# Kernel tuning notes

Hardware: AMD Instinct MI355X
Metric: run time of the kernel (lower is better)

## Reference

```python
import jax, jax.numpy as jnp
import numpy as np

B, L, S, H, C = 64, 512, 512, 768, 9  # batch, bert subword len, word seq len, hidden, num_classes


def setup_inputs() -> dict:
    key = jax.random.key(0)
    k1, k2, k3 = jax.random.split(key, 3)
    rng = np.random.RandomState(0)
    # per-word subword counts in {1,2,3}; truncate so totals fit in L subword slots
    lens = rng.randint(1, 4, size=(B, S))
    cum = lens.cumsum(axis=1)
    keep = cum <= L
    ids_lens = (lens * keep).astype(np.int32)
    totals = ids_lens.sum(axis=1)
    attention_mask = (np.arange(L)[None, :] < totals[:, None]).astype(np.int32)
    label_mask = ids_lens > 0
    label_ids = (rng.randint(0, C, size=(B, S)) * label_mask).astype(np.int32)
    bert_out = jax.random.normal(k1, (B, L, H), dtype=jnp.float32)
    W = jax.random.normal(k2, (H, C), dtype=jnp.float32) * 0.02
    b = jnp.zeros((C,), dtype=jnp.float32)
    return {
        "bert_out": bert_out,
        "W": W,
        "b": b,
        "attention_mask": jnp.asarray(attention_mask),
        "ids_lens": jnp.asarray(ids_lens),
        "label_ids": jnp.asarray(label_ids),
        "label_mask": jnp.asarray(label_mask),
    }


def reference(bert_out, W, b, attention_mask, ids_lens, label_ids, label_mask):
    Bv, Lv, Hv = bert_out.shape
    Sv = ids_lens.shape[1]
    nseg = Bv * Sv
    am = attention_mask.astype(jnp.int32)
    # subword position within each example's valid region
    sidx = jnp.cumsum(am, axis=1) - 1                       # [B, L]
    # word index for each subword: searchsorted into cumulative word lengths
    ends = jnp.cumsum(ids_lens, axis=1)                     # [B, S]
    widx = jax.vmap(lambda e, s: jnp.searchsorted(e, s, side='right'))(ends, sidx)
    seg = jnp.where(am > 0, widx + jnp.arange(Bv)[:, None] * Sv, nseg)  # pad bucket = nseg
    flat = bert_out.reshape(Bv * Lv, Hv)
    segf = seg.reshape(Bv * Lv)
    sums = jax.ops.segment_sum(flat, segf, num_segments=nseg + 1)[:nseg]
    cnts = jax.ops.segment_sum(jnp.ones((Bv * Lv,), bert_out.dtype), segf,
                               num_segments=nseg + 1)[:nseg]
    mean = sums / jnp.maximum(cnts, 1.0)[:, None]           # segment mean (split().mean(0))
    word_mask = (ids_lens > 0).reshape(nseg)
    embed = jnp.where(word_mask[:, None], mean, 0.0).reshape(Bv, Sv, Hv)  # masked_scatter
    # dropout in eval mode = identity
    logits = embed @ W + b                                  # [B, S, C]
    logp = jax.nn.log_softmax(logits, axis=-1)
    lab = jnp.clip(label_ids, 0, W.shape[1] - 1)
    nll = -jnp.take_along_axis(logp, lab[..., None].astype(jnp.int32), axis=-1)[..., 0]
    valid = label_mask.astype(bert_out.dtype)
    loss = jnp.sum(nll * valid) / jnp.maximum(jnp.sum(valid), 1.0)
    pred = jnp.argmax(logits, axis=-1)
    return loss, pred
```

## Files before the change

kernel.cpp:

```cpp
#include <hip/hip_runtime.h>
#include <math.h>

#define BB 64
#define LL 512
#define SS 512
#define HH 768
#define CC 9
#define WPV 2
#define WPB (WPV * 4)
#define GW (BB * SS / WPB)
#define NPART (GW * 4)

template <int CTRL>
__device__ __forceinline__ float dpp_add(float x) {
    int y = __builtin_amdgcn_update_dpp(0, __float_as_int(x), CTRL, 0xf, 0xf, true);
    return x + __int_as_float(y);
}
__device__ __forceinline__ float rsum64(float x) {
    x = dpp_add<0x111>(x);
    x = dpp_add<0x112>(x);
    x = dpp_add<0x114>(x);
    x = dpp_add<0x118>(x);
    x = dpp_add<0x142>(x);
    x = dpp_add<0x143>(x);
    return x;
}

__device__ __forceinline__ float4 f4add(float4 a, float4 b) {
    return make_float4(a.x + b.x, a.y + b.y, a.z + b.z, a.w + b.w);
}
__device__ __forceinline__ float dot4(float4 a, float4 b) {
    return a.x * b.x + a.y * b.y + a.z * b.z + a.w * b.w;
}

__global__ __launch_bounds__(512) void scan_wt_kernel(
    const int* __restrict__ ids_lens,
    const float* __restrict__ Wm,
    int* __restrict__ woff_g,
    float* __restrict__ WT_g)
{
    if (blockIdx.x == BB) {
        for (int e = threadIdx.x; e < HH * CC; e += 512) {
            int h = e / CC;
            int c = e - h * CC;
            WT_g[c * HH + h] = Wm[e];
        }
        return;
    }
    __shared__ int wtot[8];
    int b = blockIdx.x;
    int t = threadIdx.x, lane = t & 63, wave = t >> 6;
    int len = ids_lens[b * SS + t];
    int x = len;
#pragma unroll
    for (int off = 1; off < 64; off <<= 1) {
        int y = __shfl_up(x, off);
        if (lane >= off) x += y;
    }
    if (lane == 63) wtot[wave] = x;
    __syncthreads();
    int base = 0;
    for (int wv = 0; wv < wave; wv++) base += wtot[wv];
    woff_g[b * SS + t] = base + x - len;
}

__global__ __launch_bounds__(256, 4) void word_kernel(
    const float* __restrict__ bert,
    const float* __restrict__ WT_g,
    const float* __restrict__ bias,
    const int* __restrict__ ids_lens,
    const int* __restrict__ woff_g,
    const int* __restrict__ label_ids,
    float* __restrict__ pred_out,
    float* __restrict__ nll_part,
    float* __restrict__ cnt_part)
{
    int t = threadIdx.x, lane = t & 63, wave = t >> 6;
    int hoff = lane * 4;
    int gA = blockIdx.x * WPB + wave * WPV;
    int gB = gA + 1;
    int pid = blockIdx.x * 4 + wave;

    int lenA = ids_lens[gA];
    int lenB = ids_lens[gB];

    float bs[CC];
#pragma unroll
    for (int c = 0; c < CC; c++) bs[c] = bias[c];

    if ((lenA | lenB) == 0) {
        if (lane == 63) {
            float mx = bs[0]; int arg = 0;
#pragma unroll
            for (int c = 1; c < CC; c++) { if (bs[c] > mx) { mx = bs[c]; arg = c; } }
            pred_out[gA] = (float)arg;
            pred_out[gB] = (float)arg;
            nll_part[pid] = 0.0f;
            cnt_part[pid] = 0.0f;
        }
        return;
    }

    const float4 z4 = make_float4(0.f, 0.f, 0.f, 0.f);
    float4 PA0 = z4, PA1 = z4, PA2 = z4;
    float4 PB0 = z4, PB1 = z4, PB2 = z4;

#define LD3(dst0, dst1, dst2, base_, r_)                                         \
    do {                                                                         \
        const float* q_ = (base_) + (size_t)(r_) * HH;                           \
        dst0 = *reinterpret_cast<const float4*>(q_);                             \
        dst1 = *reinterpret_cast<const float4*>(q_ + 256);                       \
        dst2 = *reinterpret_cast<const float4*>(q_ + 512);                       \
    } while (0)

    {
        int bA = gA >> 9;
        const float* pA = bert + ((size_t)bA * LL + woff_g[gA]) * HH + hoff;
        float4 r0a, r1a, r2a, r0b, r1b, r2b, r0c, r1c, r2c;
        if (lenA > 0) LD3(r0a, r1a, r2a, pA, 0);
        if (lenA > 1) LD3(r0b, r1b, r2b, pA, 1);
        if (lenA > 2) LD3(r0c, r1c, r2c, pA, 2);
        if (lenA > 0) { PA0 = r0a; PA1 = r1a; PA2 = r2a; }
        if (lenA > 1) { PA0 = f4add(PA0, r0b); PA1 = f4add(PA1, r1b); PA2 = f4add(PA2, r2b); }
        if (lenA > 2) { PA0 = f4add(PA0, r0c); PA1 = f4add(PA1, r1c); PA2 = f4add(PA2, r2c); }
    }
    {
        int bB = gB >> 9;
        const float* pB = bert + ((size_t)bB * LL + woff_g[gB]) * HH + hoff;
        float4 r0a, r1a, r2a, r0b, r1b, r2b, r0c, r1c, r2c;
        if (lenB > 0) LD3(r0a, r1a, r2a, pB, 0);
        if (lenB > 1) LD3(r0b, r1b, r2b, pB, 1);
        if (lenB > 2) LD3(r0c, r1c, r2c, pB, 2);
        if (lenB > 0) { PB0 = r0a; PB1 = r1a; PB2 = r2a; }
        if (lenB > 1) { PB0 = f4add(PB0, r0b); PB1 = f4add(PB1, r1b); PB2 = f4add(PB2, r2b); }
        if (lenB > 2) { PB0 = f4add(PB0, r0c); PB1 = f4add(PB1, r1c); PB2 = f4add(PB2, r2c); }
    }
#undef LD3

    float accA[CC], accB[CC];
#pragma unroll
    for (int c = 0; c < CC; c++) {
        float4 w0 = *reinterpret_cast<const float4*>(WT_g + c * HH + hoff);
        float4 w1 = *reinterpret_cast<const float4*>(WT_g + c * HH + 256 + hoff);
        float4 w2 = *reinterpret_cast<const float4*>(WT_g + c * HH + 512 + hoff);
        accA[c] = dot4(PA0, w0) + dot4(PA1, w1) + dot4(PA2, w2);
        accB[c] = dot4(PB0, w0) + dot4(PB1, w1) + dot4(PB2, w2);
    }
#pragma unroll
    for (int c = 0; c < CC; c++) {
        accA[c] = rsum64(accA[c]);
        accB[c] = rsum64(accB[c]);
    }

    if (lane == 63) {
        float nll_acc = 0.0f, cnt_acc = 0.0f;
#pragma unroll
        for (int wsel = 0; wsel < 2; wsel++) {
            int g = wsel ? gB : gA;
            int len = wsel ? lenB : lenA;
            float inv = (len > 0) ? (1.0f / (float)len) : 1.0f;
            float lg[CC];
#pragma unroll
            for (int c = 0; c < CC; c++)
                lg[c] = (wsel ? accB[c] : accA[c]) * inv + bs[c];
            float mx = lg[0]; int arg = 0;
#pragma unroll
            for (int c = 1; c < CC; c++) { if (lg[c] > mx) { mx = lg[c]; arg = c; } }
            float se = 0.0f;
#pragma unroll
            for (int c = 0; c < CC; c++) se += expf(lg[c] - mx);
            float lse = mx + logf(se);
            int lab = label_ids[g];
            lab = lab < 0 ? 0 : (lab > CC - 1 ? CC - 1 : lab);
            if (len > 0) { nll_acc += lse - lg[lab]; cnt_acc += 1.0f; }
            pred_out[g] = (float)arg;
        }
        nll_part[pid] = nll_acc;
        cnt_part[pid] = cnt_acc;
    }
}

__global__ __launch_bounds__(1024) void finalize_kernel(
    const float* __restrict__ nll_part,
    const float* __restrict__ cnt_part,
    float* __restrict__ out_loss) {
    __shared__ float sn[16], sc[16];
    int t = threadIdx.x, lane = t & 63, wave = t >> 6;
    float n = 0.0f, c = 0.0f;
#pragma unroll
    for (int i = 0; i < NPART / 1024; ++i) {
        n += nll_part[t + i * 1024];
        c += cnt_part[t + i * 1024];
    }
    n = rsum64(n);
    c = rsum64(c);
    if (lane == 63) { sn[wave] = n; sc[wave] = c; }
    __syncthreads();
    if (t == 0) {
        float tn = 0.0f, tc = 0.0f;
#pragma unroll
        for (int i = 0; i < 16; i++) { tn += sn[i]; tc += sc[i]; }
        out_loss[0] = tn / fmaxf(tc, 1.0f);
    }
}

extern "C" void kernel_launch(void* const* d_in, const int* in_sizes, int n_in,
                              void* d_out, int out_size, void* d_ws, size_t ws_size,
                              hipStream_t stream) {
    const float* bert = (const float*)d_in[0];
    const float* Wm   = (const float*)d_in[1];
    const float* bias = (const float*)d_in[2];
    const int* ids_lens  = (const int*)d_in[4];
    const int* label_ids = (const int*)d_in[5];

    float* out = (float*)d_out;

    float* WT_g     = (float*)d_ws;
    int*   woff_g   = (int*)(WT_g + CC * HH);
    float* nll_part = (float*)(woff_g + BB * SS);
    float* cnt_part = nll_part + NPART;

    scan_wt_kernel<<<BB + 1, 512, 0, stream>>>(ids_lens, Wm, woff_g, WT_g);
    word_kernel<<<GW, 256, 0, stream>>>(bert, WT_g, bias, ids_lens, woff_g,
                                        label_ids, out + 1, nll_part, cnt_part);
    finalize_kernel<<<1, 1024, 0, stream>>>(nll_part, cnt_part, out);
}
```

Baseline: 179.7 us.

## Process four words per wave with H-chunked loop and scalarized offsets

Each wave now handles four words instead of two. It loops over three 256-wide hidden chunks, loading the W slice once per chunk and reusing it across all four words. Word lengths and offsets are made wave-uniform with readfirstlane so address math and branches can stay scalar. The launch-bounds occupancy hint is lowered from 4 to 3 to fit the larger per-thread accumulator state, which raises register pressure and halves the grid size.

```diff
diff --git a/kernel.cpp b/kernel.cpp
--- a/kernel.cpp
+++ b/kernel.cpp
@@ -6,7 +6,7 @@
 #define SS 512
 #define HH 768
 #define CC 9
-#define WPV 2
+#define WPV 4
 #define WPB (WPV * 4)
 #define GW (BB * SS / WPB)
 #define NPART (GW * 4)
@@ -64,7 +64,7 @@
     woff_g[b * SS + t] = base + x - len;
 }
 
-__global__ __launch_bounds__(256, 4) void word_kernel(
+__global__ __launch_bounds__(256, 3) void word_kernel(
     const float* __restrict__ bert,
     const float* __restrict__ WT_g,
     const float* __restrict__ bias,
@@ -77,92 +77,85 @@
 {
     int t = threadIdx.x, lane = t & 63, wave = t >> 6;
     int hoff = lane * 4;
-    int gA = blockIdx.x * WPB + wave * WPV;
-    int gB = gA + 1;
+    int g0 = blockIdx.x * WPB + wave * WPV;
     int pid = blockIdx.x * 4 + wave;
 
-    int lenA = ids_lens[gA];
-    int lenB = ids_lens[gB];
-
-    float bs[CC];
-#pragma unroll
-    for (int c = 0; c < CC; c++) bs[c] = bias[c];
-
-    if ((lenA | lenB) == 0) {
+    int len[WPV];
+#pragma unroll
+    for (int i = 0; i < WPV; i++)
+        len[i] = __builtin_amdgcn_readfirstlane(ids_lens[g0 + i]);
+
+    if ((len[0] | len[1] | len[2] | len[3]) == 0) {
         if (lane == 63) {
-            float mx = bs[0]; int arg = 0;
-#pragma unroll
-            for (int c = 1; c < CC; c++) { if (bs[c] > mx) { mx = bs[c]; arg = c; } }
-            pred_out[gA] = (float)arg;
-            pred_out[gB] = (float)arg;
+            float mx = bias[0]; int arg = 0;
+#pragma unroll
+            for (int c = 1; c < CC; c++) { float v = bias[c]; if (v > mx) { mx = v; arg = c; } }
+#pragma unroll
+            for (int i = 0; i < WPV; i++) pred_out[g0 + i] = (float)arg;
             nll_part[pid] = 0.0f;
             cnt_part[pid] = 0.0f;
         }
         return;
     }
 
-    const float4 z4 = make_float4(0.f, 0.f, 0.f, 0.f);
-    float4 PA0 = z4, PA1 = z4, PA2 = z4;
-    float4 PB0 = z4, PB1 = z4, PB2 = z4;
-
-#define LD3(dst0, dst1, dst2, base_, r_)                                         \
-    do {                                                                         \
-        const float* q_ = (base_) + (size_t)(r_) * HH;                           \
-        dst0 = *reinterpret_cast<const float4*>(q_);                             \
-        dst1 = *reinterpret_cast<const float4*>(q_ + 256);                       \
-        dst2 = *reinterpret_cast<const float4*>(q_ + 512);                       \
-    } while (0)
-
-    {
-        int bA = gA >> 9;
-        const float* pA = bert + ((size_t)bA * LL + woff_g[gA]) * HH + hoff;
-        float4 r0a, r1a, r2a, r0b, r1b, r2b, r0c, r1c, r2c;
-        if (lenA > 0) LD3(r0a, r1a, r2a, pA, 0);
-        if (lenA > 1) LD3(r0b, r1b, r2b, pA, 1);
-        if (lenA > 2) LD3(r0c, r1c, r2c, pA, 2);
-        if (lenA > 0) { PA0 = r0a; PA1 = r1a; PA2 = r2a; }
-        if (lenA > 1) { PA0 = f4add(PA0, r0b); PA1 = f4add(PA1, r1b); PA2 = f4add(PA2, r2b); }
-        if (lenA > 2) { PA0 = f4add(PA0, r0c); PA1 = f4add(PA1, r1c); PA2 = f4add(PA2, r2c); }
-    }
-    {
-        int bB = gB >> 9;
-        const float* pB = bert + ((size_t)bB * LL + woff_g[gB]) * HH + hoff;
-        float4 r0a, r1a, r2a, r0b, r1b, r2b, r0c, r1c, r2c;
-        if (lenB > 0) LD3(r0a, r1a, r2a, pB, 0);
-        if (lenB > 1) LD3(r0b, r1b, r2b, pB, 1);
-        if (lenB > 2) LD3(r0c, r1c, r2c, pB, 2);
-        if (lenB > 0) { PB0 = r0a; PB1 = r1a; PB2 = r2a; }
-        if (lenB > 1) { PB0 = f4add(PB0, r0b); PB1 = f4add(PB1, r1b); PB2 = f4add(PB2, r2b); }
-        if (lenB > 2) { PB0 = f4add(PB0, r0c); PB1 = f4add(PB1, r1c); PB2 = f4add(PB2, r2c); }
-    }
-#undef LD3
-
-    float accA[CC], accB[CC];
-#pragma unroll
-    for (int c = 0; c < CC; c++) {
-        float4 w0 = *reinterpret_cast<const float4*>(WT_g + c * HH + hoff);
-        float4 w1 = *reinterpret_cast<const float4*>(WT_g + c * HH + 256 + hoff);
-        float4 w2 = *reinterpret_cast<const float4*>(WT_g + c * HH + 512 + hoff);
-        accA[c] = dot4(PA0, w0) + dot4(PA1, w1) + dot4(PA2, w2);
-        accB[c] = dot4(PB0, w0) + dot4(PB1, w1) + dot4(PB2, w2);
-    }
-#pragma unroll
-    for (int c = 0; c < CC; c++) {
-        accA[c] = rsum64(accA[c]);
-        accB[c] = rsum64(accB[c]);
-    }
+    int off[WPV];
+#pragma unroll
+    for (int i = 0; i < WPV; i++)
+        off[i] = __builtin_amdgcn_readfirstlane(woff_g[g0 + i]);
+
+    int b = g0 >> 9;
+    const float* rowbase = bert + (size_t)b * LL * HH + hoff;
+
+    float acc[CC][WPV];
+#pragma unroll
+    for (int c = 0; c < CC; c++)
+#pragma unroll
+        for (int i = 0; i < WPV; i++) acc[c][i] = 0.0f;
+
+#pragma unroll
+    for (int p = 0; p < 3; p++) {
+        float4 w[CC];
+#pragma unroll
+        for (int c = 0; c < CC; c++)
+            w[c] = *reinterpret_cast<const float4*>(WT_g + c * HH + p * 256 + hoff);
+
+        float4 r0[WPV], r1[WPV], r2[WPV];
+#pragma unroll
+        for (int i = 0; i < WPV; i++) {
+            const float* q = rowbase + (size_t)off[i] * HH + p * 256;
+            if (len[i] > 0) r0[i] = *reinterpret_cast<const float4*>(q);
+            if (len[i] > 1) r1[i] = *reinterpret_cast<const float4*>(q + HH);
+            if (len[i] > 2) r2[i] = *reinterpret_cast<const float4*>(q + 2 * HH);
+        }
+
+#pragma unroll
+        for (int i = 0; i < WPV; i++) {
+            float4 s = make_float4(0.f, 0.f, 0.f, 0.f);
+            if (len[i] > 0) s = r0[i];
+            if (len[i] > 1) s = f4add(s, r1[i]);
+            if (len[i] > 2) s = f4add(s, r2[i]);
+#pragma unroll
+            for (int c = 0; c < CC; c++) acc[c][i] += dot4(s, w[c]);
+        }
+    }
+
+#pragma unroll
+    for (int c = 0; c < CC; c++)
+#pragma unroll
+        for (int i = 0; i < WPV; i++) acc[c][i] = rsum64(acc[c][i]);
 
     if (lane == 63) {
-        float nll_acc = 0.0f, cnt_acc = 0.0f;
-#pragma unroll
-        for (int wsel = 0; wsel < 2; wsel++) {
-            int g = wsel ? gB : gA;
-            int len = wsel ? lenB : lenA;
-            float inv = (len > 0) ? (1.0f / (float)len) : 1.0f;
+        float bs[CC];
+#pragma unroll
+        for (int c = 0; c < CC; c++) bs[c] = bias[c];
+        float nll = 0.0f, cnt = 0.0f;
+#pragma unroll
+        for (int i = 0; i < WPV; i++) {
+            int ln = len[i];
+            float inv = (ln > 0) ? (1.0f / (float)ln) : 1.0f;
             float lg[CC];
 #pragma unroll
-            for (int c = 0; c < CC; c++)
-                lg[c] = (wsel ? accB[c] : accA[c]) * inv + bs[c];
+            for (int c = 0; c < CC; c++) lg[c] = acc[c][i] * inv + bs[c];
             float mx = lg[0]; int arg = 0;
 #pragma unroll
             for (int c = 1; c < CC; c++) { if (lg[c] > mx) { mx = lg[c]; arg = c; } }
@@ -170,13 +163,14 @@
 #pragma unroll
             for (int c = 0; c < CC; c++) se += expf(lg[c] - mx);
             float lse = mx + logf(se);
+            int g = g0 + i;
             int lab = label_ids[g];
             lab = lab < 0 ? 0 : (lab > CC - 1 ? CC - 1 : lab);
-            if (len > 0) { nll_acc += lse - lg[lab]; cnt_acc += 1.0f; }
+            if (ln > 0) { nll += lse - lg[lab]; cnt += 1.0f; }
             pred_out[g] = (float)arg;
         }
-        nll_part[pid] = nll_acc;
-        cnt_part[pid] = cnt_acc;
+        nll_part[pid] = nll;
+        cnt_part[pid] = cnt;
     }
 }
 
```

After: 259.3 us. +44.3%, slower.
